# Kernel optimization log

Measured on AMD Instinct MI355X. Metric: run time of the kernel, lower is better.

## Reference

```python
import jax, jax.numpy as jnp
import numpy as np

NUM_HEADS = 24
HEAD_DIM = 64
SCALE = HEAD_DIM ** -0.5


def setup_inputs() -> dict:
    key = jax.random.key(0)
    ks = jax.random.split(key, 6)
    b, n_img, n_txt = 2, 4096, 128
    c_in, c_out, c_ctx = 1536, 1536, 4096
    x = jax.random.normal(ks[0], (b, n_img, c_in), dtype=jnp.float32)
    context = jax.random.normal(ks[1], (b, n_txt, c_ctx), dtype=jnp.float32)
    # realistic padding mask: first 96 of 128 tokens valid
    context_mask = jnp.broadcast_to(jnp.arange(n_txt) < 96, (b, n_txt))
    # Linear(in, out, bias=False) stored as [in, out] so y = x @ W
    Wq = jax.random.normal(ks[2], (c_in, c_out), dtype=jnp.float32) * (c_in ** -0.5)
    Wk = jax.random.normal(ks[3], (c_ctx, c_out), dtype=jnp.float32) * (c_ctx ** -0.5)
    Wv = jax.random.normal(ks[4], (c_ctx, c_out), dtype=jnp.float32) * (c_ctx ** -0.5)
    Wo = jax.random.normal(ks[5], (c_out, c_out), dtype=jnp.float32) * (c_out ** -0.5)
    return {"x": x, "context": context, "context_mask": context_mask,
            "Wq": Wq, "Wk": Wk, "Wv": Wv, "Wo": Wo}


def reference(x, context, context_mask, Wq, Wk, Wv, Wo):
    b, n, _ = x.shape
    h, d = NUM_HEADS, HEAD_DIM
    # project and split heads: b n (h d) -> b h n d
    q = (x @ Wq).reshape(b, n, h, d).transpose(0, 2, 1, 3)
    k = (context @ Wk).reshape(b, -1, h, d).transpose(0, 2, 1, 3)
    v = (context @ Wv).reshape(b, -1, h, d).transpose(0, 2, 1, 3)
    scores = jnp.einsum('bhid,bhjd->bhij', q, k) * SCALE
    max_neg = -jnp.finfo(scores.dtype).max
    scores = jnp.where(context_mask[:, None, None, :], scores, max_neg)
    attn = jax.nn.softmax(scores, axis=-1)
    out = jnp.einsum('bhij,bhjd->bhid', attn, v)
    out = out.transpose(0, 2, 1, 3).reshape(b, n, h * d)
    return out @ Wo
```

## Files before the change

kernel.cpp:

```cpp
#include <hip/hip_runtime.h>

typedef __attribute__((ext_vector_type(8))) short s8bf;
typedef __attribute__((ext_vector_type(8))) __bf16 v8bf;
typedef __attribute__((ext_vector_type(4))) float f32x4;

__device__ __forceinline__ short f2bf(float f) {
  union { float f; unsigned u; } v; v.f = f;
  unsigned r = v.u + 0x7FFFu + ((v.u >> 16) & 1u);
  return (short)(r >> 16);
}

__device__ __forceinline__ s8bf pack8(float4 a, float4 b) {
  s8bf o;
  o[0] = f2bf(a.x); o[1] = f2bf(a.y); o[2] = f2bf(a.z); o[3] = f2bf(a.w);
  o[4] = f2bf(b.x); o[5] = f2bf(b.y); o[6] = f2bf(b.z); o[7] = f2bf(b.w);
  return o;
}

__device__ __forceinline__ f32x4 mfma16(s8bf a, s8bf b, f32x4 c) {
  return __builtin_amdgcn_mfma_f32_16x16x32_bf16(
      __builtin_bit_cast(v8bf, a), __builtin_bit_cast(v8bf, b), c, 0, 0, 0);
}

__device__ __forceinline__ void gl_lds16(const void* g, void* l) {
  __builtin_amdgcn_global_load_lds(
      (const __attribute__((address_space(1))) unsigned*)g,
      (__attribute__((address_space(3))) unsigned*)l, 16, 0, 0);
}

__global__ __launch_bounds__(256) void cast_k(
    const float* __restrict__ x, const float* __restrict__ ctx,
    const void* __restrict__ msk,
    short* __restrict__ xbf, short* __restrict__ ctxbf, float* __restrict__ bias)
{
  __shared__ int fmt;
  const int blk = blockIdx.x;
  const int t = threadIdx.x;
  if (blk < 1664) {
    const float4* src;
    s8bf* dst;
    if (blk < 1536) { src = (const float4*)x + (size_t)blk * 2048;
                      dst = (s8bf*)xbf + (size_t)blk * 1024; }
    else            { src = (const float4*)ctx + (size_t)(blk - 1536) * 2048;
                      dst = (s8bf*)ctxbf + (size_t)(blk - 1536) * 1024; }
    float4 a0 = src[2 * t];        float4 b0 = src[2 * t + 1];
    float4 a1 = src[2 * t + 512];  float4 b1 = src[2 * t + 513];
    float4 a2 = src[2 * t + 1024]; float4 b2 = src[2 * t + 1025];
    float4 a3 = src[2 * t + 1536]; float4 b3 = src[2 * t + 1537];
    dst[t]       = pack8(a0, b0);
    dst[t + 256] = pack8(a1, b1);
    dst[t + 512] = pack8(a2, b2);
    dst[t + 768] = pack8(a3, b3);
  } else {
    const unsigned char* p8 = (const unsigned char*)msk;
    if (t == 0) {
      const float* pf = (const float*)msk;
      int allf = 1, anyone = 0;
      for (int i = 0; i < 64; ++i) {
        float f = pf[i];
        if (f != 0.0f && f != 1.0f) allf = 0;
        if (f == 1.0f) anyone = 1;
      }
      int any13 = 0;
      for (int i = 0; i < 256; ++i) if ((i & 3) && p8[i]) any13 = 1;
      fmt = (allf && anyone) ? 2 : (any13 ? 0 : 1);
    }
    __syncthreads();
    int j = t;
    if (j < 256) {
      int m;
      if (fmt == 2)      m = (((const float*)msk)[j] != 0.0f);
      else if (fmt == 0) m = (p8[j] != 0);
      else               m = (((const int*)msk)[j] != 0);
      bias[j] = m ? 0.0f : -1e30f;
    }
  }
}

__global__ __launch_bounds__(256) void transp_k(
    const float* __restrict__ Wq, const float* __restrict__ Wk,
    const float* __restrict__ Wv, const float* __restrict__ Wo,
    short* __restrict__ WqT, short* __restrict__ WkT,
    short* __restrict__ WvT, short* __restrict__ WoT)
{
  __shared__ float tile[64][65];
  int t = blockIdx.x;
  const float* W; short* Wt; int K, t0;
  if (t < 576)       { W = Wq; Wt = WqT; K = 1536; t0 = t; }
  else if (t < 2112) { W = Wk; Wt = WkT; K = 4096; t0 = t - 576; }
  else if (t < 3648) { W = Wv; Wt = WvT; K = 4096; t0 = t - 2112; }
  else               { W = Wo; Wt = WoT; K = 1536; t0 = t - 3648; }
  const int N = 1536;
  int ntx = K / 64;
  int k0 = (t0 % ntx) * 64, n0 = (t0 / ntx) * 64;
  int r = threadIdx.x >> 4;
  int c4 = threadIdx.x & 15;
  #pragma unroll
  for (int i = 0; i < 4; ++i) {
    float4 v = *(const float4*)(W + (size_t)(k0 + r + i * 16) * N + n0 + c4 * 4);
    tile[r + i * 16][c4 * 4 + 0] = v.x;
    tile[r + i * 16][c4 * 4 + 1] = v.y;
    tile[r + i * 16][c4 * 4 + 2] = v.z;
    tile[r + i * 16][c4 * 4 + 3] = v.w;
  }
  __syncthreads();
  int n = threadIdx.x >> 3, kc = threadIdx.x & 7;
  #pragma unroll
  for (int half = 0; half < 2; ++half) {
    int nn = n + half * 32;
    s8bf o;
    #pragma unroll
    for (int j = 0; j < 8; ++j) o[j] = f2bf(tile[kc * 8 + j][nn]);
    *(s8bf*)(Wt + (size_t)(n0 + nn) * K + k0 + kc * 8) = o;
  }
}

template<int MODE>
__global__ __launch_bounds__(512, 2) void gemm4ph_k(
    const short* __restrict__ A, const short* __restrict__ Bt, void* __restrict__ C,
    int M, int N, int K)
{
  extern __shared__ char ldsb[];
  const int tid = threadIdx.x, wid = tid >> 6, lane = tid & 63;
  const int nbx = N / 192;
  const int nwg = gridDim.x, bid = blockIdx.x;
  const int swz = (bid & 7) * (nwg >> 3) + (bid >> 3);
  const int m0 = (swz / nbx) * 256, n0 = (swz % nbx) * 192;
  const int wm = wid >> 2, wn = wid & 3;
  const int NT = K / 64;

  const int l = lane & 15, h = lane >> 4;
  const int rdslot = (((l & 1) * 4 + h) ^ (l >> 1)) * 16;
  int aoff[8], boff[3];
  #pragma unroll
  for (int mf = 0; mf < 8; ++mf)
    aoff[mf] = (wm * 64 + mf * 8 + (l >> 1)) * 128 + rdslot;
  #pragma unroll
  for (int nf = 0; nf < 3; ++nf)
    boff[nf] = 32768 + (wn * 24 + nf * 8 + (l >> 1)) * 128 + rdslot;

  const int ls = (tid & 7) ^ ((tid >> 3) & 7);
  const int srow2 = 2 * (tid >> 3) + (ls >> 2);
  const int scol = (ls & 3) * 8;
  const short* sA_lo = A  + (size_t)(m0 + srow2) * K + scol;
  const short* sA_hi = A  + (size_t)(m0 + 128 + srow2) * K + scol;
  const short* sB_lo = Bt + (size_t)(n0 + srow2) * K + scol;
  const short* sB_hi = Bt + (size_t)(n0 + 128 + srow2) * K + scol;
  const int d16 = tid * 16;

  f32x4 acc[8][3] = {};
  s8bf av[4], av2[4], bk[3];

  gl_lds16(sA_lo,      ldsb + 0     + d16);
  gl_lds16(sA_hi,      ldsb + 8192  + d16);
  gl_lds16(sB_lo,      ldsb + 32768 + d16);
  if (wid < 4) gl_lds16(sB_hi,      ldsb + 40960 + d16);
  gl_lds16(sA_lo + 32, ldsb + 16384 + d16);
  gl_lds16(sA_hi + 32, ldsb + 24576 + d16);
  gl_lds16(sB_lo + 32, ldsb + 45056 + d16);
  if (wid < 4) gl_lds16(sB_hi + 32, ldsb + 53248 + d16);
  gl_lds16(sA_lo + 64, ldsb + 57344 + 0     + d16);
  gl_lds16(sA_hi + 64, ldsb + 57344 + 8192  + d16);
  gl_lds16(sB_lo + 64, ldsb + 57344 + 32768 + d16);
  if (wid < 4) gl_lds16(sB_hi + 64, ldsb + 57344 + 40960 + d16);
  if (wid < 4) asm volatile("s_waitcnt vmcnt(8)" ::: "memory");
  else         asm volatile("s_waitcnt vmcnt(6)" ::: "memory");
  __builtin_amdgcn_s_barrier();

  for (int t = 0; t < NT; ++t) {
    const int bo = (t & 1) * 57344, bo2 = bo ^ 57344;
    const int kt1 = ((t + 1) < NT ? (t + 1) : (NT - 1)) * 64;
    const int kt2 = ((t + 2) < NT ? (t + 2) : (NT - 1)) * 64;
    #pragma unroll
    for (int i = 0; i < 4; ++i) av[i] = *(const s8bf*)(ldsb + bo + aoff[i]);
    #pragma unroll
    for (int nf = 0; nf < 3; ++nf) bk[nf] = *(const s8bf*)(ldsb + bo + boff[nf]);
    gl_lds16(sA_lo + kt1 + 32, ldsb + bo2 + 16384 + d16);
    gl_lds16(sA_hi + kt1 + 32, ldsb + bo2 + 24576 + d16);
    __builtin_amdgcn_s_barrier();
    asm volatile("s_waitcnt lgkmcnt(0)" ::: "memory");
    __builtin_amdgcn_s_setprio(1);
    #pragma unroll
    for (int i = 0; i < 4; ++i)
      #pragma unroll
      for (int nf = 0; nf < 3; ++nf)
        acc[i][nf] = mfma16(av[i], bk[nf], acc[i][nf]);
    __builtin_amdgcn_s_setprio(0);
    __builtin_amdgcn_s_barrier();
    #pragma unroll
    for (int i = 0; i < 4; ++i) av2[i] = *(const s8bf*)(ldsb + bo + aoff[4 + i]);
    gl_lds16(sB_lo + kt1 + 32, ldsb + bo2 + 45056 + d16);
    if (wid < 4) gl_lds16(sB_hi + kt1 + 32, ldsb + bo2 + 53248 + d16);
    __builtin_amdgcn_s_barrier();
    asm volatile("s_waitcnt lgkmcnt(0)" ::: "memory");
    __builtin_amdgcn_s_setprio(1);
    #pragma unroll
    for (int i = 0; i < 4; ++i)
      #pragma unroll
      for (int nf = 0; nf < 3; ++nf)
        acc[4 + i][nf] = mfma16(av2[i], bk[nf], acc[4 + i][nf]);
    __builtin_amdgcn_s_setprio(0);
    if (wid < 4) asm volatile("s_waitcnt vmcnt(8)" ::: "memory");
    else         asm volatile("s_waitcnt vmcnt(6)" ::: "memory");
    __builtin_amdgcn_s_barrier();
    #pragma unroll
    for (int i = 0; i < 4; ++i) av[i] = *(const s8bf*)(ldsb + bo + 16384 + aoff[i]);
    #pragma unroll
    for (int nf = 0; nf < 3; ++nf) bk[nf] = *(const s8bf*)(ldsb + bo + 12288 + boff[nf]);
    gl_lds16(sA_lo + kt2, ldsb + bo + 0    + d16);
    gl_lds16(sA_hi + kt2, ldsb + bo + 8192 + d16);
    __builtin_amdgcn_s_barrier();
    asm volatile("s_waitcnt lgkmcnt(0)" ::: "memory");
    __builtin_amdgcn_s_setprio(1);
    #pragma unroll
    for (int i = 0; i < 4; ++i)
      #pragma unroll
      for (int nf = 0; nf < 3; ++nf)
        acc[i][nf] = mfma16(av[i], bk[nf], acc[i][nf]);
    __builtin_amdgcn_s_setprio(0);
    __builtin_amdgcn_s_barrier();
    #pragma unroll
    for (int i = 0; i < 4; ++i) av2[i] = *(const s8bf*)(ldsb + bo + 16384 + aoff[4 + i]);
    gl_lds16(sB_lo + kt2, ldsb + bo + 32768 + d16);
    if (wid < 4) gl_lds16(sB_hi + kt2, ldsb + bo + 40960 + d16);
    __builtin_amdgcn_s_barrier();
    asm volatile("s_waitcnt lgkmcnt(0)" ::: "memory");
    __builtin_amdgcn_s_setprio(1);
    #pragma unroll
    for (int i = 0; i < 4; ++i)
      #pragma unroll
      for (int nf = 0; nf < 3; ++nf)
        acc[4 + i][nf] = mfma16(av2[i], bk[nf], acc[4 + i][nf]);
    __builtin_amdgcn_s_setprio(0);
    if (wid < 4) asm volatile("s_waitcnt vmcnt(8)" ::: "memory");
    else         asm volatile("s_waitcnt vmcnt(6)" ::: "memory");
    __builtin_amdgcn_s_barrier();
  }
  asm volatile("s_waitcnt vmcnt(0)" ::: "memory");

  const int r0 = m0 + wm * 128 + ((lane >> 4) << 2);
  const int c0 = n0 + wn * 48 + (lane & 15);
  #pragma unroll
  for (int mf = 0; mf < 8; ++mf)
    #pragma unroll
    for (int nf = 0; nf < 3; ++nf)
      #pragma unroll
      for (int v = 0; v < 4; ++v) {
        int row = r0 + mf * 16 + v, col = c0 + nf * 16;
        float val = acc[mf][nf][v];
        if (MODE == 0) ((short*)C)[(size_t)row * N + col] = f2bf(val);
        else           ((float*)C)[(size_t)row * N + col] = val;
      }
}

template<int MODE>
__global__ __launch_bounds__(256, 2) void gemm_bt_k(
    const short* __restrict__ A, const short* __restrict__ Bt, void* __restrict__ C,
    int M, int N, int K, int kchunk)
{
  __shared__ short aT[128 * 32];
  __shared__ short bT[128 * 32];
  const int m0 = blockIdx.x * 128, n0 = blockIdx.y * 128;
  const int wid = threadIdx.x >> 6, lane = threadIdx.x & 63;
  const int wr = wid >> 1, wc = wid & 1;
  const int k_lo = blockIdx.z * kchunk, k_hi = k_lo + kchunk;
  f32x4 acc[4][4] = {};
  const int srow = wid * 32 + (lane >> 2);
  const int skoff = (lane & 3) * 8;
  const short* aG = A + (size_t)(m0 + srow) * K + skoff;
  const short* bG = Bt + (size_t)(n0 + srow) * K + skoff;
  char* aL = (char*)aT + wid * 2048;
  char* bL = (char*)bT + wid * 2048;
  const short* ap = aT + (wr * 64 + (lane & 15)) * 32 + (lane >> 4) * 8;
  const short* bp = bT + (wc * 64 + (lane & 15)) * 32 + (lane >> 4) * 8;
  for (int k0 = k_lo; k0 < k_hi; k0 += 32) {
    gl_lds16(aG + k0, aL);
    gl_lds16(aG + (size_t)16 * K + k0, aL + 1024);
    gl_lds16(bG + k0, bL);
    gl_lds16(bG + (size_t)16 * K + k0, bL + 1024);
    __syncthreads();
    s8bf af[4], bf[4];
    #pragma unroll
    for (int i = 0; i < 4; ++i) {
      af[i] = *(const s8bf*)(ap + i * 512);
      bf[i] = *(const s8bf*)(bp + i * 512);
    }
    #pragma unroll
    for (int mi = 0; mi < 4; ++mi)
      #pragma unroll
      for (int ni = 0; ni < 4; ++ni)
        acc[mi][ni] = mfma16(af[mi], bf[ni], acc[mi][ni]);
    __syncthreads();
  }
  const int r0 = m0 + wr * 64 + ((lane >> 4) << 2);
  const int c0 = n0 + wc * 64 + (lane & 15);
  float* Cf = (float*)C + (size_t)blockIdx.z * 786432;
  #pragma unroll
  for (int mi = 0; mi < 4; ++mi)
    #pragma unroll
    for (int ni = 0; ni < 4; ++ni)
      #pragma unroll
      for (int v = 0; v < 4; ++v) {
        int row = r0 + mi * 16 + v, col = c0 + ni * 16;
        Cf[(size_t)row * N + col] = acc[mi][ni][v];
      }
}

__global__ void kv_reduce_k(const float* __restrict__ part, short* __restrict__ kbf,
                            short* __restrict__ vtbf) {
  int t = blockIdx.x * 256 + threadIdx.x;
  int row = t / 768, c4 = (t % 768) * 4;
  float4 s = {0.f, 0.f, 0.f, 0.f};
  const float* p = part + (size_t)row * 3072 + c4;
  #pragma unroll
  for (int z = 0; z < 4; ++z) {
    float4 v = *(const float4*)(p + (size_t)z * 786432);
    s.x += v.x; s.y += v.y; s.z += v.z; s.w += v.w;
  }
  if (c4 < 1536) {
    short4 o = { f2bf(s.x), f2bf(s.y), f2bf(s.z), f2bf(s.w) };
    *(short4*)(kbf + (size_t)row * 1536 + c4) = o;
  } else {
    int b = row >> 7, j = row & 127, c = c4 - 1536;
    vtbf[((size_t)(b * 1536 + c + 0)) * 128 + j] = f2bf(s.x);
    vtbf[((size_t)(b * 1536 + c + 1)) * 128 + j] = f2bf(s.y);
    vtbf[((size_t)(b * 1536 + c + 2)) * 128 + j] = f2bf(s.z);
    vtbf[((size_t)(b * 1536 + c + 3)) * 128 + j] = f2bf(s.w);
  }
}

__global__ __launch_bounds__(256, 3) void attn_k(
    const short* __restrict__ q, const short* __restrict__ kk,
    const short* __restrict__ vt, const float* __restrict__ bias,
    short* __restrict__ ao)
{
  __shared__ char sm_[49152];
  const int it = blockIdx.x, h = blockIdx.y, b = blockIdx.z;
  const int wid = threadIdx.x >> 6, lane = threadIdx.x & 63;
  const int i0 = it * 128;
  char* kT = sm_;
  char* vT = sm_ + 16384;
  char* pB = (wid < 2) ? (sm_ + wid * 8192) : (sm_ + 16384 + wid * 8192);

  #pragma unroll
  for (int c = 0; c < 4; ++c) {
    int seg = c * 256 + wid * 64 + lane;
    int j = seg >> 3, ds = seg & 7;
    int dsrc = ds ^ (j & 7);
    gl_lds16(kk + ((size_t)(b * 128 + j) * 1536 + h * 64 + dsrc * 8),
             kT + c * 4096 + wid * 1024);
  }
  #pragma unroll
  for (int c = 0; c < 4; ++c) {
    int seg = c * 256 + wid * 64 + lane;
    int d = seg >> 4, js = seg & 15;
    int jsrc = js ^ (d & 7);
    gl_lds16(vt + ((size_t)(b * 1536 + h * 64 + d) * 128 + jsrc * 8),
             vT + c * 4096 + wid * 1024);
  }

  float bcol[8];
  #pragma unroll
  for (int nj = 0; nj < 8; ++nj) bcol[nj] = bias[b * 128 + nj * 16 + (lane & 15)];

  s8bf qf[2][2];
  #pragma unroll
  for (int mi = 0; mi < 2; ++mi)
    #pragma unroll
    for (int ks = 0; ks < 2; ++ks) {
      size_t row = (size_t)(b * 4096 + i0 + wid * 32 + mi * 16 + (lane & 15));
      qf[mi][ks] = *(const s8bf*)(q + row * 1536 + h * 64 + ks * 32 + (lane >> 4) * 8);
    }
  __syncthreads();

  f32x4 s[2][8] = {};
  #pragma unroll
  for (int ks = 0; ks < 2; ++ks) {
    int kd = ks * 32 + (lane >> 4) * 8;
    #pragma unroll
    for (int nj = 0; nj < 8; ++nj) {
      int j = nj * 16 + (lane & 15);
      s8bf kb = *(const s8bf*)(kT + j * 128 + ((2 * kd) ^ ((j & 7) << 4)));
      s[0][nj] = mfma16(qf[0][ks], kb, s[0][nj]);
      s[1][nj] = mfma16(qf[1][ks], kb, s[1][nj]);
    }
  }
  __syncthreads();

  float sm[2][4];
  #pragma unroll
  for (int mi = 0; mi < 2; ++mi)
    #pragma unroll
    for (int v = 0; v < 4; ++v) {
      float mx = -1e30f;
      #pragma unroll
      for (int nj = 0; nj < 8; ++nj) {
        float sv = s[mi][nj][v] * 0.125f + bcol[nj];
        s[mi][nj][v] = sv;
        mx = fmaxf(mx, sv);
      }
      mx = fmaxf(mx, __shfl_xor(mx, 1));
      mx = fmaxf(mx, __shfl_xor(mx, 2));
      mx = fmaxf(mx, __shfl_xor(mx, 4));
      mx = fmaxf(mx, __shfl_xor(mx, 8));
      float ss = 0.f;
      #pragma unroll
      for (int nj = 0; nj < 8; ++nj) {
        float p = __expf(s[mi][nj][v] - mx);
        s[mi][nj][v] = p;
        ss += p;
      }
      ss += __shfl_xor(ss, 1);
      ss += __shfl_xor(ss, 2);
      ss += __shfl_xor(ss, 4);
      ss += __shfl_xor(ss, 8);
      sm[mi][v] = ss;
    }

  #pragma unroll
  for (int mi = 0; mi < 2; ++mi)
    #pragma unroll
    for (int v = 0; v < 4; ++v) {
      int r = mi * 16 + ((lane >> 4) << 2) + v;
      char* base = pB + r * 256;
      #pragma unroll
      for (int nj = 0; nj < 8; ++nj) {
        int j = nj * 16 + (lane & 15);
        *(short*)(base + ((2 * j) ^ ((r & 7) << 4))) = f2bf(s[mi][nj][v]);
      }
    }
  __syncthreads();

  f32x4 o_[2][4] = {};
  #pragma unroll
  for (int ks = 0; ks < 4; ++ks) {
    int j = ks * 32 + (lane >> 4) * 8;
    s8bf pa[2];
    #pragma unroll
    for (int mi = 0; mi < 2; ++mi) {
      int r = mi * 16 + (lane & 15);
      pa[mi] = *(const s8bf*)(pB + r * 256 + ((2 * j) ^ ((r & 7) << 4)));
    }
    #pragma unroll
    for (int dj = 0; dj < 4; ++dj) {
      int d = dj * 16 + (lane & 15);
      s8bf vb = *(const s8bf*)(vT + d * 256 + ((2 * j) ^ ((d & 7) << 4)));
      o_[0][dj] = mfma16(pa[0], vb, o_[0][dj]);
      o_[1][dj] = mfma16(pa[1], vb, o_[1][dj]);
    }
  }

  #pragma unroll
  for (int mi = 0; mi < 2; ++mi)
    #pragma unroll
    for (int v = 0; v < 4; ++v) {
      int r = mi * 16 + ((lane >> 4) << 2) + v;
      float is = 1.0f / sm[mi][v];
      size_t row = (size_t)(b * 4096 + i0 + wid * 32 + r);
      #pragma unroll
      for (int dj = 0; dj < 4; ++dj) {
        int d = dj * 16 + (lane & 15);
        ao[row * 1536 + h * 64 + d] = f2bf(o_[mi][dj][v] * is);
      }
    }
}

extern "C" void kernel_launch(void* const* d_in, const int* in_sizes, int n_in,
                              void* d_out, int out_size, void* d_ws, size_t ws_size,
                              hipStream_t stream) {
  const float* x   = (const float*)d_in[0];
  const float* ctx = (const float*)d_in[1];
  const void*  msk = d_in[2];
  const float* Wq  = (const float*)d_in[3];
  const float* Wk  = (const float*)d_in[4];
  const float* Wv  = (const float*)d_in[5];
  const float* Wo  = (const float*)d_in[6];
  float* out = (float*)d_out;

  const int B = 2, NI = 4096, NT = 128, C = 1536, CC = 4096, H = 24;
  const int Mq = B * NI;
  const int Mk = B * NT;

  size_t off = 0;
  auto carve = [&](size_t bytes) -> void* {
    void* p = (char*)d_ws + off;
    off += (bytes + 255) & ~(size_t)255;
    return p;
  };
  short* xbf   = (short*)carve((size_t)Mq * C * 2);
  short* ctxbf = (short*)carve((size_t)Mk * CC * 2);
  short* WqT   = (short*)carve((size_t)C * C * 2);
  short* WkT   = (short*)carve((size_t)CC * C * 2);
  short* WvT   = (short*)carve((size_t)CC * C * 2);
  short* WoT   = (short*)carve((size_t)C * C * 2);
  short* qbf   = (short*)carve((size_t)Mq * C * 2);
  short* kbf   = (short*)carve((size_t)Mk * C * 2);
  short* vtbf  = (short*)carve((size_t)Mk * C * 2);
  float* bias  = (float*)carve(256 * 4);
  short* aout  = xbf;
  float* part  = out;

  hipFuncSetAttribute((const void*)gemm4ph_k<0>, hipFuncAttributeMaxDynamicSharedMemorySize, 114688);
  hipFuncSetAttribute((const void*)gemm4ph_k<1>, hipFuncAttributeMaxDynamicSharedMemorySize, 114688);

  cast_k<<<1665, 256, 0, stream>>>(x, ctx, msk, xbf, ctxbf, bias);
  transp_k<<<4224, 256, 0, stream>>>(Wq, Wk, Wv, Wo, WqT, WkT, WvT, WoT);

  gemm4ph_k<0><<<(Mq / 256) * (C / 192), 512, 114688, stream>>>(xbf, WqT, qbf, Mq, C, C);
  gemm_bt_k<5><<<dim3(Mk / 128, 3072 / 128, 4), 256, 0, stream>>>(ctxbf, WkT, part, Mk, 3072, CC, 1024);
  kv_reduce_k<<<768, 256, 0, stream>>>(part, kbf, vtbf);

  attn_k<<<dim3(NI / 128, H, B), 256, 0, stream>>>(qbf, kbf, vtbf, bias, aout);

  gemm4ph_k<1><<<(Mq / 256) * (C / 192), 512, 114688, stream>>>(aout, WoT, out, Mq, C, C);
}
```

Measured before the change: 170.8 us.

## Replace 4-phase 256x192 GEMM with smaller 128x192 two-stage pipelined GEMM

The Q and output projection GEMMs move from a 512-thread, 256x192-tile kernel with a four-phase K=64 schedule to a 256-thread, 128x192-tile kernel. The new kernel uses K=32 steps with a simple double-buffered LDS pipeline, one barrier per step and 40KB of LDS. This targets occupancy (3 blocks per CU) and a grid twice as large, so the 8192x1536 output fills the CUs better and the scheduling is simpler. In exchange each block loads more A/B data per FLOP, gets less reuse, and has fewer MFMAs per barrier to hide latency.

```diff
diff --git a/kernel.cpp b/kernel.cpp
--- a/kernel.cpp
+++ b/kernel.cpp
@@ -116,7 +116,7 @@
 }
 
 template<int MODE>
-__global__ __launch_bounds__(512, 2) void gemm4ph_k(
+__global__ __launch_bounds__(256, 3) void gemm2ph_k(
     const short* __restrict__ A, const short* __restrict__ Bt, void* __restrict__ C,
     int M, int N, int K)
 {
@@ -125,121 +125,69 @@
   const int nbx = N / 192;
   const int nwg = gridDim.x, bid = blockIdx.x;
   const int swz = (bid & 7) * (nwg >> 3) + (bid >> 3);
-  const int m0 = (swz / nbx) * 256, n0 = (swz % nbx) * 192;
-  const int wm = wid >> 2, wn = wid & 3;
-  const int NT = K / 64;
+  const int m0 = (swz / nbx) * 128, n0 = (swz % nbx) * 192;
+  const int NT = K / 32;
 
   const int l = lane & 15, h = lane >> 4;
   const int rdslot = (((l & 1) * 4 + h) ^ (l >> 1)) * 16;
   int aoff[8], boff[3];
   #pragma unroll
   for (int mf = 0; mf < 8; ++mf)
-    aoff[mf] = (wm * 64 + mf * 8 + (l >> 1)) * 128 + rdslot;
+    aoff[mf] = (mf * 8 + (l >> 1)) * 128 + rdslot;
   #pragma unroll
   for (int nf = 0; nf < 3; ++nf)
-    boff[nf] = 32768 + (wn * 24 + nf * 8 + (l >> 1)) * 128 + rdslot;
+    boff[nf] = 8192 + (wid * 24 + nf * 8 + (l >> 1)) * 128 + rdslot;
 
   const int ls = (tid & 7) ^ ((tid >> 3) & 7);
   const int srow2 = 2 * (tid >> 3) + (ls >> 2);
   const int scol = (ls & 3) * 8;
-  const short* sA_lo = A  + (size_t)(m0 + srow2) * K + scol;
-  const short* sA_hi = A  + (size_t)(m0 + 128 + srow2) * K + scol;
-  const short* sB_lo = Bt + (size_t)(n0 + srow2) * K + scol;
-  const short* sB_hi = Bt + (size_t)(n0 + 128 + srow2) * K + scol;
+  const short* sA0 = A  + (size_t)(m0 + srow2) * K + scol;
+  const short* sA1 = A  + (size_t)(m0 + 64 + srow2) * K + scol;
+  const short* sB0 = Bt + (size_t)(n0 + srow2) * K + scol;
+  const short* sB1 = Bt + (size_t)(n0 + 64 + srow2) * K + scol;
+  const short* sB2 = Bt + (size_t)(n0 + 128 + srow2) * K + scol;
   const int d16 = tid * 16;
 
+  auto stage = [&](int ko, int bo_) {
+    gl_lds16(sA0 + ko, ldsb + bo_ + 0     + d16);
+    gl_lds16(sA1 + ko, ldsb + bo_ + 4096  + d16);
+    gl_lds16(sB0 + ko, ldsb + bo_ + 8192  + d16);
+    gl_lds16(sB1 + ko, ldsb + bo_ + 12288 + d16);
+    gl_lds16(sB2 + ko, ldsb + bo_ + 16384 + d16);
+  };
+
   f32x4 acc[8][3] = {};
-  s8bf av[4], av2[4], bk[3];
-
-  gl_lds16(sA_lo,      ldsb + 0     + d16);
-  gl_lds16(sA_hi,      ldsb + 8192  + d16);
-  gl_lds16(sB_lo,      ldsb + 32768 + d16);
-  if (wid < 4) gl_lds16(sB_hi,      ldsb + 40960 + d16);
-  gl_lds16(sA_lo + 32, ldsb + 16384 + d16);
-  gl_lds16(sA_hi + 32, ldsb + 24576 + d16);
-  gl_lds16(sB_lo + 32, ldsb + 45056 + d16);
-  if (wid < 4) gl_lds16(sB_hi + 32, ldsb + 53248 + d16);
-  gl_lds16(sA_lo + 64, ldsb + 57344 + 0     + d16);
-  gl_lds16(sA_hi + 64, ldsb + 57344 + 8192  + d16);
-  gl_lds16(sB_lo + 64, ldsb + 57344 + 32768 + d16);
-  if (wid < 4) gl_lds16(sB_hi + 64, ldsb + 57344 + 40960 + d16);
-  if (wid < 4) asm volatile("s_waitcnt vmcnt(8)" ::: "memory");
-  else         asm volatile("s_waitcnt vmcnt(6)" ::: "memory");
+  s8bf a[8], bk[3];
+
+  stage(0, 0);
+  stage(((1 < NT) ? 1 : 0) * 32, 20480);
+  asm volatile("s_waitcnt vmcnt(5)" ::: "memory");
   __builtin_amdgcn_s_barrier();
 
   for (int t = 0; t < NT; ++t) {
-    const int bo = (t & 1) * 57344, bo2 = bo ^ 57344;
-    const int kt1 = ((t + 1) < NT ? (t + 1) : (NT - 1)) * 64;
-    const int kt2 = ((t + 2) < NT ? (t + 2) : (NT - 1)) * 64;
-    #pragma unroll
-    for (int i = 0; i < 4; ++i) av[i] = *(const s8bf*)(ldsb + bo + aoff[i]);
+    const int bo = (t & 1) * 20480;
+    const int kt2 = ((t + 2) < NT ? (t + 2) : (NT - 1)) * 32;
+    #pragma unroll
+    for (int mf = 0; mf < 8; ++mf) a[mf] = *(const s8bf*)(ldsb + bo + aoff[mf]);
     #pragma unroll
     for (int nf = 0; nf < 3; ++nf) bk[nf] = *(const s8bf*)(ldsb + bo + boff[nf]);
-    gl_lds16(sA_lo + kt1 + 32, ldsb + bo2 + 16384 + d16);
-    gl_lds16(sA_hi + kt1 + 32, ldsb + bo2 + 24576 + d16);
+    asm volatile("s_waitcnt lgkmcnt(0)" ::: "memory");
     __builtin_amdgcn_s_barrier();
-    asm volatile("s_waitcnt lgkmcnt(0)" ::: "memory");
+    stage(kt2, bo);
     __builtin_amdgcn_s_setprio(1);
     #pragma unroll
-    for (int i = 0; i < 4; ++i)
+    for (int mf = 0; mf < 8; ++mf)
       #pragma unroll
       for (int nf = 0; nf < 3; ++nf)
-        acc[i][nf] = mfma16(av[i], bk[nf], acc[i][nf]);
+        acc[mf][nf] = mfma16(a[mf], bk[nf], acc[mf][nf]);
     __builtin_amdgcn_s_setprio(0);
+    asm volatile("s_waitcnt vmcnt(5)" ::: "memory");
     __builtin_amdgcn_s_barrier();
-    #pragma unroll
-    for (int i = 0; i < 4; ++i) av2[i] = *(const s8bf*)(ldsb + bo + aoff[4 + i]);
-    gl_lds16(sB_lo + kt1 + 32, ldsb + bo2 + 45056 + d16);
-    if (wid < 4) gl_lds16(sB_hi + kt1 + 32, ldsb + bo2 + 53248 + d16);
-    __builtin_amdgcn_s_barrier();
-    asm volatile("s_waitcnt lgkmcnt(0)" ::: "memory");
-    __builtin_amdgcn_s_setprio(1);
-    #pragma unroll
-    for (int i = 0; i < 4; ++i)
-      #pragma unroll
-      for (int nf = 0; nf < 3; ++nf)
-        acc[4 + i][nf] = mfma16(av2[i], bk[nf], acc[4 + i][nf]);
-    __builtin_amdgcn_s_setprio(0);
-    if (wid < 4) asm volatile("s_waitcnt vmcnt(8)" ::: "memory");
-    else         asm volatile("s_waitcnt vmcnt(6)" ::: "memory");
-    __builtin_amdgcn_s_barrier();
-    #pragma unroll
-    for (int i = 0; i < 4; ++i) av[i] = *(const s8bf*)(ldsb + bo + 16384 + aoff[i]);
-    #pragma unroll
-    for (int nf = 0; nf < 3; ++nf) bk[nf] = *(const s8bf*)(ldsb + bo + 12288 + boff[nf]);
-    gl_lds16(sA_lo + kt2, ldsb + bo + 0    + d16);
-    gl_lds16(sA_hi + kt2, ldsb + bo + 8192 + d16);
-    __builtin_amdgcn_s_barrier();
-    asm volatile("s_waitcnt lgkmcnt(0)" ::: "memory");
-    __builtin_amdgcn_s_setprio(1);
-    #pragma unroll
-    for (int i = 0; i < 4; ++i)
-      #pragma unroll
-      for (int nf = 0; nf < 3; ++nf)
-        acc[i][nf] = mfma16(av[i], bk[nf], acc[i][nf]);
-    __builtin_amdgcn_s_setprio(0);
-    __builtin_amdgcn_s_barrier();
-    #pragma unroll
-    for (int i = 0; i < 4; ++i) av2[i] = *(const s8bf*)(ldsb + bo + 16384 + aoff[4 + i]);
-    gl_lds16(sB_lo + kt2, ldsb + bo + 32768 + d16);
-    if (wid < 4) gl_lds16(sB_hi + kt2, ldsb + bo + 40960 + d16);
-    __builtin_amdgcn_s_barrier();
-    asm volatile("s_waitcnt lgkmcnt(0)" ::: "memory");
-    __builtin_amdgcn_s_setprio(1);
-    #pragma unroll
-    for (int i = 0; i < 4; ++i)
-      #pragma unroll
-      for (int nf = 0; nf < 3; ++nf)
-        acc[4 + i][nf] = mfma16(av2[i], bk[nf], acc[4 + i][nf]);
-    __builtin_amdgcn_s_setprio(0);
-    if (wid < 4) asm volatile("s_waitcnt vmcnt(8)" ::: "memory");
-    else         asm volatile("s_waitcnt vmcnt(6)" ::: "memory");
-    __builtin_amdgcn_s_barrier();
   }
   asm volatile("s_waitcnt vmcnt(0)" ::: "memory");
 
-  const int r0 = m0 + wm * 128 + ((lane >> 4) << 2);
-  const int c0 = n0 + wn * 48 + (lane & 15);
+  const int r0 = m0 + ((lane >> 4) << 2);
+  const int c0 = n0 + wid * 48 + (lane & 15);
   #pragma unroll
   for (int mf = 0; mf < 8; ++mf)
     #pragma unroll
@@ -500,17 +448,17 @@
   short* aout  = xbf;
   float* part  = out;
 
-  hipFuncSetAttribute((const void*)gemm4ph_k<0>, hipFuncAttributeMaxDynamicSharedMemorySize, 114688);
-  hipFuncSetAttribute((const void*)gemm4ph_k<1>, hipFuncAttributeMaxDynamicSharedMemorySize, 114688);
+  hipFuncSetAttribute((const void*)gemm2ph_k<0>, hipFuncAttributeMaxDynamicSharedMemorySize, 40960);
+  hipFuncSetAttribute((const void*)gemm2ph_k<1>, hipFuncAttributeMaxDynamicSharedMemorySize, 40960);
 
   cast_k<<<1665, 256, 0, stream>>>(x, ctx, msk, xbf, ctxbf, bias);
   transp_k<<<4224, 256, 0, stream>>>(Wq, Wk, Wv, Wo, WqT, WkT, WvT, WoT);
 
-  gemm4ph_k<0><<<(Mq / 256) * (C / 192), 512, 114688, stream>>>(xbf, WqT, qbf, Mq, C, C);
+  gemm2ph_k<0><<<(Mq / 128) * (C / 192), 256, 40960, stream>>>(xbf, WqT, qbf, Mq, C, C);
   gemm_bt_k<5><<<dim3(Mk / 128, 3072 / 128, 4), 256, 0, stream>>>(ctxbf, WkT, part, Mk, 3072, CC, 1024);
   kv_reduce_k<<<768, 256, 0, stream>>>(part, kbf, vtbf);
 
   attn_k<<<dim3(NI / 128, H, B), 256, 0, stream>>>(qbf, kbf, vtbf, bias, aout);
 
-  gemm4ph_k<1><<<(Mq / 256) * (C / 192), 512, 114688, stream>>>(aout, WoT, out, Mq, C, C);
-}
+  gemm2ph_k<1><<<(Mq / 128) * (C / 192), 256, 40960, stream>>>(aout, WoT, out, Mq, C, C);
+}
```

Result: slower. 178.9 us (+4.7%).
